# Kernel tuning notes

Measured on AMD Instinct MI355X. Metric: run time of the kernel, lower is better.

Reference implementation:

```python
import jax, jax.numpy as jnp
import numpy as np

DZ, DB, DS, DX, BATCH, T = 128, 32, 32, 64, 64, 4096


def setup_inputs() -> dict:
    # AW initialized as in PLRNN.init_AW: eye + (1/dz^2) M M^T, spectral norm 1
    rng = np.random.default_rng(0)
    M = rng.standard_normal((DZ, DZ)).astype(np.float32)
    A = np.eye(DZ, dtype=np.float32) + (M @ M.T) / (DZ * DZ)
    A = A / np.max(np.abs(np.linalg.eigvals(A)))
    AW = jnp.asarray(0.95 * A, dtype=jnp.float32)  # 0.95 margin keeps long rollout stable

    key = jax.random.key(0)
    ks = jax.random.split(key, 7)
    z0 = jax.random.normal(ks[0], (BATCH, DZ), dtype=jnp.float32)
    inputs = jax.random.normal(ks[1], (T, DS), dtype=jnp.float32)
    h = 0.1 * jax.random.normal(ks[2], (DZ,), dtype=jnp.float32)
    thetas = 2.0 * jax.random.normal(ks[3], (DZ, DB), dtype=jnp.float32) - 1.0
    alphas = 2.0 * jax.random.normal(ks[4], (DB,), dtype=jnp.float32) - 1.0
    clipping = 5.0 * jnp.ones((DZ, DB), dtype=jnp.float32)  # fixed buffer in torch
    C = 0.1 * jax.random.normal(ks[5], (DZ, DS), dtype=jnp.float32)
    B_obs = jax.random.normal(ks[6], (DZ, DX), dtype=jnp.float32)
    return dict(z0=z0, inputs=inputs, AW=AW, h=h, thetas=thetas,
                alphas=alphas, clipping=clipping, C=C, B_obs=B_obs)


def _leaky(x):
    # nn.LeakyReLU(0.18)
    return jnp.where(x >= 0, x, 0.18 * x)


def reference(z0, inputs, AW, h, thetas, alphas, clipping, C, B_obs):
    # split_diag_offdiag: A = diag(AW), W = AW - diag(AW)
    a_diag = jnp.diag(AW)            # (dz,)
    W = AW - jnp.diag(a_diag)        # (dz, dz), zero diagonal

    def step(z, s):
        # z: (B, dz), s: (ds,)
        d = z[:, :, None] - thetas   # (B, dz, db)
        be = (jnp.sum(alphas * _leaky(d), axis=-1)
              - jnp.sum(alphas * _leaky(d + clipping), axis=-1))  # (B, dz)
        z_new = z * a_diag + be @ W.T + h + (C @ s)  # diag matmul == elementwise
        return z_new, z_new

    _, Z = jax.lax.scan(step, z0, inputs)   # (T, B, dz)
    # torch.cat over list of (B, dz) -> (T*B, dz), time-major
    Z = Z.reshape(-1, Z.shape[-1])
    return Z @ B_obs                        # linear_observation: (T*B, dx)
```

## Files before the change

kernel.cpp:

```cpp
#include <hip/hip_runtime.h>
#include <hip/hip_bf16.h>
#include <hip/hip_fp16.h>

#define DZ 128
#define DB 32
#define DSIN 32
#define DX 64
#define NB 64
#define TT 4096

typedef short v8s __attribute__((ext_vector_type(8)));
typedef float v4f __attribute__((ext_vector_type(4)));
typedef _Float16 v2h __attribute__((ext_vector_type(2)));

__device__ __forceinline__ float dpp_xor1(float x) {
  int y = __builtin_amdgcn_mov_dpp(__builtin_bit_cast(int, x), 0xB1, 0xF, 0xF, true);
  return __builtin_bit_cast(float, y);
}
__device__ __forceinline__ float dpp_xor2(float x) {
  int y = __builtin_amdgcn_mov_dpp(__builtin_bit_cast(int, x), 0x4E, 0xF, 0xF, true);
  return __builtin_bit_cast(float, y);
}

__device__ __forceinline__ short f2bf(float f) {
  __hip_bfloat16 h = __float2bfloat16(f);
  return *reinterpret_cast<short*>(&h);
}

__device__ __forceinline__ v2h pk2h(float a, float b) {
  return __builtin_bit_cast(v2h, __builtin_amdgcn_cvt_pkrtz(a, b));
}
__device__ __forceinline__ float fdot2(v2h a, v2h b, float c) {
  return __builtin_amdgcn_fdot2(a, b, c, false);
}

__global__ void k_prep(const float* __restrict__ AW, const float* __restrict__ alphas,
                       const float* __restrict__ clip, float* __restrict__ WCd) {
  __shared__ float cd[DZ];
  int j = threadIdx.x;
  float s = 0.f;
  for (int k = 0; k < DB; ++k) s = fmaf(alphas[k], clip[j * DB + k], s);
  cd[j] = s;
  __syncthreads();
  float acc = 0.f;
  for (int jj = 0; jj < DZ; ++jj)
    if (jj != j) acc = fmaf(AW[j * DZ + jj], cd[jj], acc);
  WCd[j] = acc;
}

__global__ void k_u(const float* __restrict__ inp, const float* __restrict__ h,
                    const float* __restrict__ C, const float* __restrict__ WCd,
                    float* __restrict__ UT) {
  int gid = blockIdx.x * blockDim.x + threadIdx.x;
  int i = gid >> 10;
  int t0 = (gid & 1023) * 4;
  float base = h[i] - WCd[i];
  const float4* c4 = (const float4*)(C + i * DSIN);
  float4 cv[8];
#pragma unroll
  for (int s = 0; s < 8; ++s) cv[s] = c4[s];
  float out[4];
#pragma unroll
  for (int tt = 0; tt < 4; ++tt) {
    const float4* i4 = (const float4*)(inp + (size_t)(t0 + tt) * DSIN);
    float u = base;
#pragma unroll
    for (int s = 0; s < 8; ++s) {
      float4 iv = i4[s];
      u = fmaf(cv[s].x, iv.x, u);
      u = fmaf(cv[s].y, iv.y, u);
      u = fmaf(cv[s].z, iv.z, u);
      u = fmaf(cv[s].w, iv.w, u);
    }
    out[tt] = u;
  }
  *(float4*)(UT + (size_t)i * TT + t0) = make_float4(out[0], out[1], out[2], out[3]);
}

__global__ __launch_bounds__(512, 1) void k_scan(
    const float* __restrict__ z0, const float* __restrict__ AW,
    const float* __restrict__ thetas, const float* __restrict__ alphas,
    const float* __restrict__ clip, const float* __restrict__ UT,
    short* __restrict__ Z) {
  __shared__ __align__(16) _Float16 gsh[2][DZ];
  const int b = blockIdx.x;
  const int tid = threadIdx.x;
  const int i = tid >> 2, s = tid & 3;
  const int c0 = 32 * s;

  v2h w[16];
#pragma unroll
  for (int j = 0; j < 16; ++j) {
    float2 a = *(const float2*)(AW + (size_t)i * DZ + c0 + 2 * j);
    float x = (c0 + 2 * j == i) ? 0.f : a.x;
    float y = (c0 + 2 * j + 1 == i) ? 0.f : a.y;
    w[j] = pk2h(x, y);
  }
  const float adiag = AW[(size_t)i * DZ + i];

  v2h th[4], nc[4], al[4];
#pragma unroll
  for (int m = 0; m < 4; ++m) {
    int k = 8 * s + 2 * m;
    th[m] = pk2h(thetas[i * DB + k], thetas[i * DB + k + 1]);
    nc[m] = pk2h(-clip[i * DB + k], -clip[i * DB + k + 1]);
    al[m] = pk2h(-0.82f * alphas[k], -0.82f * alphas[k + 1]);
  }

  float z = z0[b * DZ + i];
  const float4* up = (const float4*)(UT + (size_t)i * TT);
  float4 ug = up[0];
  short* zp = Z + b * DZ + i;
  const v2h zero2 = pk2h(0.f, 0.f);

#pragma unroll 1
  for (int tg = 0; tg < TT / 4; ++tg) {
    float4 ugn = up[(tg + 1 < TT / 4) ? tg + 1 : tg];
    float uarr[4] = {ug.x, ug.y, ug.z, ug.w};
#pragma unroll
    for (int q = 0; q < 4; ++q) {
      _Float16* gq = gsh[q & 1];
      v2h z2 = pk2h(z, z);
      float g0 = 0.f, g1 = 0.f;
#pragma unroll
      for (int m = 0; m < 4; m += 2) {
        v2h d0 = __builtin_elementwise_min(
            __builtin_elementwise_max(z2 - th[m], nc[m]), zero2);
        v2h d1 = __builtin_elementwise_min(
            __builtin_elementwise_max(z2 - th[m + 1], nc[m + 1]), zero2);
        g0 = fdot2(al[m], d0, g0);
        g1 = fdot2(al[m + 1], d1, g1);
      }
      float gf = g0 + g1;
      gf += dpp_xor1(gf);
      gf += dpp_xor2(gf);
      _Float16 ghalf = (_Float16)gf;
      if (s == 0) gq[i] = ghalf;
      asm volatile("s_waitcnt lgkmcnt(0)\n\ts_barrier" ::: "memory");

      const uint4* g4 = ((const uint4*)gq) + 4 * s;
      float m0 = 0.f, m1 = 0.f, m2 = 0.f, m3 = 0.f;
#pragma unroll
      for (int r = 0; r < 4; ++r) {
        uint4 qd = g4[r];
        m0 = fdot2(w[4 * r + 0], __builtin_bit_cast(v2h, qd.x), m0);
        m1 = fdot2(w[4 * r + 1], __builtin_bit_cast(v2h, qd.y), m1);
        m2 = fdot2(w[4 * r + 2], __builtin_bit_cast(v2h, qd.z), m2);
        m3 = fdot2(w[4 * r + 3], __builtin_bit_cast(v2h, qd.w), m3);
      }
      float mm = (m0 + m1) + (m2 + m3);
      mm += dpp_xor1(mm);
      mm += dpp_xor2(mm);
      z = fmaf(z, adiag, mm + uarr[q]);
      if (s == 0) zp[(size_t)(tg * 4 + q) * (NB * DZ)] = f2bf(z);
    }
    ug = ugn;
  }
}

__global__ __launch_bounds__(256) void k_obs(const short* __restrict__ Z,
                                             const float* __restrict__ Bo,
                                             float* __restrict__ out) {
  const int lane = threadIdx.x & 63;
  const int wv = threadIdx.x >> 6;
  const int rl = lane & 15;
  const int g = lane >> 4;

  v8s bfr[4][4];
#pragma unroll
  for (int nt = 0; nt < 4; ++nt) {
#pragma unroll
    for (int ks = 0; ks < 4; ++ks) {
      v8s f;
#pragma unroll
      for (int m = 0; m < 8; ++m) {
        int k = ks * 32 + g * 8 + m;
        f[m] = f2bf(Bo[k * DX + nt * 16 + rl]);
      }
      bfr[nt][ks] = f;
    }
  }

#pragma unroll
  for (int it = 0; it < 4; ++it) {
    const int r0 = blockIdx.x * 256 + it * 64 + wv * 16;
    const short* zrow = Z + (size_t)(r0 + rl) * DZ;
    v8s afr[4];
#pragma unroll
    for (int ks = 0; ks < 4; ++ks)
      afr[ks] = *(const v8s*)(zrow + ks * 32 + g * 8);
    v4f acc[4];
#pragma unroll
    for (int nt = 0; nt < 4; ++nt) acc[nt] = (v4f){0.f, 0.f, 0.f, 0.f};
#pragma unroll
    for (int nt = 0; nt < 4; ++nt) {
#pragma unroll
      for (int ks = 0; ks < 4; ++ks)
        acc[nt] = __builtin_amdgcn_mfma_f32_16x16x32_bf16(afr[ks], bfr[nt][ks], acc[nt], 0, 0, 0);
    }
#pragma unroll
    for (int nt = 0; nt < 4; ++nt) {
#pragma unroll
      for (int q = 0; q < 4; ++q)
        out[(size_t)(r0 + g * 4 + q) * DX + nt * 16 + rl] = acc[nt][q];
    }
  }
}

extern "C" void kernel_launch(void* const* d_in, const int* in_sizes, int n_in,
                              void* d_out, int out_size, void* d_ws, size_t ws_size,
                              hipStream_t stream) {
  const float* z0 = (const float*)d_in[0];
  const float* inp = (const float*)d_in[1];
  const float* AW = (const float*)d_in[2];
  const float* h = (const float*)d_in[3];
  const float* thetas = (const float*)d_in[4];
  const float* alphas = (const float*)d_in[5];
  const float* clip = (const float*)d_in[6];
  const float* C = (const float*)d_in[7];
  const float* Bo = (const float*)d_in[8];
  float* out = (float*)d_out;

  char* ws = (char*)d_ws;
  float* WCd = (float*)ws;
  float* UT = (float*)(ws + 1024);
  short* Z = (short*)(ws + 1024 + (size_t)TT * DZ * 4);

  k_prep<<<1, 128, 0, stream>>>(AW, alphas, clip, WCd);
  k_u<<<(DZ * TT / 4) / 256, 256, 0, stream>>>(inp, h, C, WCd, UT);
  k_scan<<<NB, 512, 0, stream>>>(z0, AW, thetas, alphas, clip, UT, Z);
  k_obs<<<(TT * NB) / 256, 256, 0, stream>>>(Z, Bo, out);
}
```

Baseline: 1.462 ms.

## Process two state rows per thread in scan, halving block to 256 threads

Each thread group of four lanes now handles two adjacent state dimensions instead of one, so the scan block drops from 512 to 256 threads (4 waves instead of 8). Shared-memory activations are written as packed half2 pairs and Z is stored as packed bf16 pairs via v_cvt_pk_bf16_f32. The aim is to make the per-step barrier cheaper with fewer waves and to gain more ILP per thread. In exchange each thread does twice the serial ALU work per step and holds twice the registers.

Result: slower. 1.635 ms (+11.8%).

```diff
diff --git a/kernel.cpp b/kernel.cpp
--- a/kernel.cpp
+++ b/kernel.cpp
@@ -25,6 +25,12 @@
 __device__ __forceinline__ short f2bf(float f) {
   __hip_bfloat16 h = __float2bfloat16(f);
   return *reinterpret_cast<short*>(&h);
+}
+
+__device__ __forceinline__ unsigned cvt_pk_bf16(float lo, float hi) {
+  unsigned r;
+  asm volatile("v_cvt_pk_bf16_f32 %0, %1, %2" : "=v"(r) : "v"(lo), "v"(hi));
+  return r;
 }
 
 __device__ __forceinline__ v2h pk2h(float a, float b) {
@@ -77,84 +83,111 @@
   *(float4*)(UT + (size_t)i * TT + t0) = make_float4(out[0], out[1], out[2], out[3]);
 }
 
-__global__ __launch_bounds__(512, 1) void k_scan(
+__global__ __launch_bounds__(256, 1) void k_scan(
     const float* __restrict__ z0, const float* __restrict__ AW,
     const float* __restrict__ thetas, const float* __restrict__ alphas,
     const float* __restrict__ clip, const float* __restrict__ UT,
-    short* __restrict__ Z) {
-  __shared__ __align__(16) _Float16 gsh[2][DZ];
+    unsigned* __restrict__ Z32) {
+  __shared__ __align__(16) unsigned gpk[2][64];
   const int b = blockIdx.x;
   const int tid = threadIdx.x;
-  const int i = tid >> 2, s = tid & 3;
+  const int p = tid >> 2, s = tid & 3;
+  const int i0 = 2 * p, i1 = i0 + 1;
   const int c0 = 32 * s;
 
-  v2h w[16];
+  v2h w0[16], w1[16];
 #pragma unroll
   for (int j = 0; j < 16; ++j) {
-    float2 a = *(const float2*)(AW + (size_t)i * DZ + c0 + 2 * j);
-    float x = (c0 + 2 * j == i) ? 0.f : a.x;
-    float y = (c0 + 2 * j + 1 == i) ? 0.f : a.y;
-    w[j] = pk2h(x, y);
-  }
-  const float adiag = AW[(size_t)i * DZ + i];
-
-  v2h th[4], nc[4], al[4];
+    float2 a0 = *(const float2*)(AW + (size_t)i0 * DZ + c0 + 2 * j);
+    float2 a1 = *(const float2*)(AW + (size_t)i1 * DZ + c0 + 2 * j);
+    bool dg = (c0 + 2 * j == i0);
+    w0[j] = pk2h(dg ? 0.f : a0.x, a0.y);
+    w1[j] = pk2h(a1.x, dg ? 0.f : a1.y);
+  }
+  const float ad0 = AW[(size_t)i0 * DZ + i0], ad1 = AW[(size_t)i1 * DZ + i1];
+
+  v2h th0[4], th1[4], nc0[4], nc1[4], al[4];
 #pragma unroll
   for (int m = 0; m < 4; ++m) {
     int k = 8 * s + 2 * m;
-    th[m] = pk2h(thetas[i * DB + k], thetas[i * DB + k + 1]);
-    nc[m] = pk2h(-clip[i * DB + k], -clip[i * DB + k + 1]);
+    th0[m] = pk2h(thetas[i0 * DB + k], thetas[i0 * DB + k + 1]);
+    th1[m] = pk2h(thetas[i1 * DB + k], thetas[i1 * DB + k + 1]);
+    nc0[m] = pk2h(-clip[i0 * DB + k], -clip[i0 * DB + k + 1]);
+    nc1[m] = pk2h(-clip[i1 * DB + k], -clip[i1 * DB + k + 1]);
     al[m] = pk2h(-0.82f * alphas[k], -0.82f * alphas[k + 1]);
   }
 
-  float z = z0[b * DZ + i];
-  const float4* up = (const float4*)(UT + (size_t)i * TT);
-  float4 ug = up[0];
-  short* zp = Z + b * DZ + i;
+  float zA = z0[b * DZ + i0], zB = z0[b * DZ + i1];
+  const float4* upA = (const float4*)(UT + (size_t)i0 * TT);
+  const float4* upB = (const float4*)(UT + (size_t)i1 * TT);
+  float4 ugA = upA[0], ugB = upB[0];
+  unsigned* zp = Z32 + (size_t)b * 64 + p;
   const v2h zero2 = pk2h(0.f, 0.f);
 
 #pragma unroll 1
   for (int tg = 0; tg < TT / 4; ++tg) {
-    float4 ugn = up[(tg + 1 < TT / 4) ? tg + 1 : tg];
-    float uarr[4] = {ug.x, ug.y, ug.z, ug.w};
+    int tn = (tg + 1 < TT / 4) ? tg + 1 : tg;
+    float4 ugAn = upA[tn], ugBn = upB[tn];
+    float uA[4] = {ugA.x, ugA.y, ugA.z, ugA.w};
+    float uB[4] = {ugB.x, ugB.y, ugB.z, ugB.w};
 #pragma unroll
     for (int q = 0; q < 4; ++q) {
-      _Float16* gq = gsh[q & 1];
-      v2h z2 = pk2h(z, z);
-      float g0 = 0.f, g1 = 0.f;
+      unsigned* gq = gpk[q & 1];
+      v2h zA2 = pk2h(zA, zA), zB2 = pk2h(zB, zB);
+      float gA0 = 0.f, gA1 = 0.f, gB0 = 0.f, gB1 = 0.f;
 #pragma unroll
       for (int m = 0; m < 4; m += 2) {
-        v2h d0 = __builtin_elementwise_min(
-            __builtin_elementwise_max(z2 - th[m], nc[m]), zero2);
-        v2h d1 = __builtin_elementwise_min(
-            __builtin_elementwise_max(z2 - th[m + 1], nc[m + 1]), zero2);
-        g0 = fdot2(al[m], d0, g0);
-        g1 = fdot2(al[m + 1], d1, g1);
+        v2h dA0 = __builtin_elementwise_min(
+            __builtin_elementwise_max(zA2 - th0[m], nc0[m]), zero2);
+        v2h dA1 = __builtin_elementwise_min(
+            __builtin_elementwise_max(zA2 - th0[m + 1], nc0[m + 1]), zero2);
+        v2h dB0 = __builtin_elementwise_min(
+            __builtin_elementwise_max(zB2 - th1[m], nc1[m]), zero2);
+        v2h dB1 = __builtin_elementwise_min(
+            __builtin_elementwise_max(zB2 - th1[m + 1], nc1[m + 1]), zero2);
+        gA0 = fdot2(al[m], dA0, gA0);
+        gA1 = fdot2(al[m + 1], dA1, gA1);
+        gB0 = fdot2(al[m], dB0, gB0);
+        gB1 = fdot2(al[m + 1], dB1, gB1);
       }
-      float gf = g0 + g1;
-      gf += dpp_xor1(gf);
-      gf += dpp_xor2(gf);
-      _Float16 ghalf = (_Float16)gf;
-      if (s == 0) gq[i] = ghalf;
+      float gA = gA0 + gA1;
+      gA += dpp_xor1(gA);
+      gA += dpp_xor2(gA);
+      float gB = gB0 + gB1;
+      gB += dpp_xor1(gB);
+      gB += dpp_xor2(gB);
+      if (s == 0) gq[p] = __builtin_bit_cast(unsigned, pk2h(gA, gB));
       asm volatile("s_waitcnt lgkmcnt(0)\n\ts_barrier" ::: "memory");
 
       const uint4* g4 = ((const uint4*)gq) + 4 * s;
-      float m0 = 0.f, m1 = 0.f, m2 = 0.f, m3 = 0.f;
+      float mA0 = 0.f, mA1 = 0.f, mA2 = 0.f, mA3 = 0.f;
+      float mB0 = 0.f, mB1 = 0.f, mB2 = 0.f, mB3 = 0.f;
 #pragma unroll
       for (int r = 0; r < 4; ++r) {
         uint4 qd = g4[r];
-        m0 = fdot2(w[4 * r + 0], __builtin_bit_cast(v2h, qd.x), m0);
-        m1 = fdot2(w[4 * r + 1], __builtin_bit_cast(v2h, qd.y), m1);
-        m2 = fdot2(w[4 * r + 2], __builtin_bit_cast(v2h, qd.z), m2);
-        m3 = fdot2(w[4 * r + 3], __builtin_bit_cast(v2h, qd.w), m3);
+        v2h q0 = __builtin_bit_cast(v2h, qd.x), q1 = __builtin_bit_cast(v2h, qd.y);
+        v2h q2 = __builtin_bit_cast(v2h, qd.z), q3 = __builtin_bit_cast(v2h, qd.w);
+        mA0 = fdot2(w0[4 * r + 0], q0, mA0);
+        mA1 = fdot2(w0[4 * r + 1], q1, mA1);
+        mA2 = fdot2(w0[4 * r + 2], q2, mA2);
+        mA3 = fdot2(w0[4 * r + 3], q3, mA3);
+        mB0 = fdot2(w1[4 * r + 0], q0, mB0);
+        mB1 = fdot2(w1[4 * r + 1], q1, mB1);
+        mB2 = fdot2(w1[4 * r + 2], q2, mB2);
+        mB3 = fdot2(w1[4 * r + 3], q3, mB3);
       }
-      float mm = (m0 + m1) + (m2 + m3);
-      mm += dpp_xor1(mm);
-      mm += dpp_xor2(mm);
-      z = fmaf(z, adiag, mm + uarr[q]);
-      if (s == 0) zp[(size_t)(tg * 4 + q) * (NB * DZ)] = f2bf(z);
-    }
-    ug = ugn;
+      float mA = (mA0 + mA1) + (mA2 + mA3);
+      mA += dpp_xor1(mA);
+      mA += dpp_xor2(mA);
+      float mB = (mB0 + mB1) + (mB2 + mB3);
+      mB += dpp_xor1(mB);
+      mB += dpp_xor2(mB);
+      zA = fmaf(zA, ad0, mA + uA[q]);
+      zB = fmaf(zB, ad1, mB + uB[q]);
+      if (s == 0) zp[(size_t)(tg * 4 + q) * (NB * 64)] = cvt_pk_bf16(zA, zB);
+    }
+    ugA = ugAn;
+    ugB = ugBn;
   }
 }
 
@@ -228,6 +261,6 @@
 
   k_prep<<<1, 128, 0, stream>>>(AW, alphas, clip, WCd);
   k_u<<<(DZ * TT / 4) / 256, 256, 0, stream>>>(inp, h, C, WCd, UT);
-  k_scan<<<NB, 512, 0, stream>>>(z0, AW, thetas, alphas, clip, UT, Z);
+  k_scan<<<NB, 256, 0, stream>>>(z0, AW, thetas, alphas, clip, UT, (unsigned*)Z);
   k_obs<<<(TT * NB) / 256, 256, 0, stream>>>(Z, Bo, out);
 }
```
